# Optimization experiments

Measured on AMD Instinct MI355X. Metric: run time of the kernel, lower is better.

Reference implementation:

```python
import jax, jax.numpy as jnp
import numpy as np

N = 50000   # nodes
E = 800000  # edges (before self loops)
NEG_SLOPE = 0.2
EPS_BN = 1e-5
EPS_SM = 1e-16  # PyG softmax denominator epsilon


def gat_conv(x, src, dst, W, att_src, att_dst, bias, heads, ch):
    n = x.shape[0]
    xh = (x @ W).reshape(n, heads, ch)                       # [N,H,C]
    a_src = jnp.sum(xh * att_src, axis=-1)                   # [N,H]
    a_dst = jnp.sum(xh * att_dst, axis=-1)                   # [N,H]
    e = a_src[src] + a_dst[dst]                              # [E,H]
    e = jax.nn.leaky_relu(e, NEG_SLOPE)
    m = jax.ops.segment_max(e, dst, num_segments=n)          # segment softmax
    ex = jnp.exp(e - m[dst])
    denom = jax.ops.segment_sum(ex, dst, num_segments=n)
    alpha = ex / (denom[dst] + EPS_SM)                       # [E,H]
    msg = alpha[:, :, None] * xh[src]                        # [E,H,C]
    out = jax.ops.segment_sum(msg, dst, num_segments=n)      # [N,H,C]
    return out.reshape(n, heads * ch) + bias


def batch_norm(x, gamma, beta):
    mu = jnp.mean(x, axis=0)
    var = jnp.mean((x - mu) ** 2, axis=0)
    return (x - mu) * jax.lax.rsqrt(var + EPS_BN) * gamma + beta


def setup_inputs() -> dict:
    key = jax.random.key(0)
    ks = jax.random.split(key, 16)
    d = {}
    d['x'] = jax.random.normal(ks[0], (N, 128), jnp.float32)
    d['edge_index'] = jax.random.randint(ks[1], (2, E), 0, N, dtype=jnp.int64)
    d['W1'] = jax.random.normal(ks[2], (128, 256), jnp.float32) * 0.1
    d['as1'] = jax.random.normal(ks[3], (2, 128), jnp.float32) * 0.1
    d['ad1'] = jax.random.normal(ks[4], (2, 128), jnp.float32) * 0.1
    d['b1'] = jax.random.normal(ks[5], (256,), jnp.float32) * 0.1
    d['g1'] = jnp.ones((256,), jnp.float32)
    d['be1'] = jnp.zeros((256,), jnp.float32)
    d['W2'] = jax.random.normal(ks[6], (256, 128), jnp.float32) * 0.1
    d['as2'] = jax.random.normal(ks[7], (2, 64), jnp.float32) * 0.1
    d['ad2'] = jax.random.normal(ks[8], (2, 64), jnp.float32) * 0.1
    d['b2'] = jax.random.normal(ks[9], (128,), jnp.float32) * 0.1
    d['g2'] = jnp.ones((128,), jnp.float32)
    d['be2'] = jnp.zeros((128,), jnp.float32)
    d['W3'] = jax.random.normal(ks[10], (128, 128), jnp.float32) * 0.1
    d['as3'] = jax.random.normal(ks[11], (2, 64), jnp.float32) * 0.1
    d['ad3'] = jax.random.normal(ks[12], (2, 64), jnp.float32) * 0.1
    d['b3'] = jax.random.normal(ks[13], (128,), jnp.float32) * 0.1
    d['lw'] = jax.random.normal(ks[14], (128, 64), jnp.float32) * 0.1
    d['lb'] = jnp.zeros((64,), jnp.float32)
    return d


def reference(x, edge_index, W1, as1, ad1, b1, g1, be1,
              W2, as2, ad2, b2, g2, be2,
              W3, as3, ad3, b3, lw, lb):
    # add self loops (PyG GATConv default add_self_loops=True)
    loops = jnp.arange(N, dtype=edge_index.dtype)
    src = jnp.concatenate([edge_index[0], loops])
    dst = jnp.concatenate([edge_index[1], loops])

    h = jax.nn.relu(gat_conv(x, src, dst, W1, as1, ad1, b1, 2, 128))   # [N,256]
    h = batch_norm(h, g1, be1)
    h = jax.nn.relu(gat_conv(h, src, dst, W2, as2, ad2, b2, 2, 64))    # [N,128]
    h = batch_norm(h, g2, be2)
    h = jax.nn.relu(gat_conv(h, src, dst, W3, as3, ad3, b3, 2, 64))    # [N,128]
    return h @ lw + lb                                                 # [N,64]
```

## Files before the change

kernel.cpp:

```cpp
#include <hip/hip_runtime.h>
#include <hip/hip_bf16.h>

#define NEG_SLOPE 0.2f
#define EPS_BN 1e-5f
#define EPS_SM 1e-16f
#define CAP 128

typedef __bf16 bf16x8 __attribute__((ext_vector_type(8)));
typedef __bf16 bf16x4 __attribute__((ext_vector_type(4)));
typedef float floatx4 __attribute__((ext_vector_type(4)));

__device__ __forceinline__ float leaky(float x) { return x > 0.f ? x : NEG_SLOPE * x; }

__global__ void k_init(const int* __restrict__ ei, int* __restrict__ flag,
                       int* __restrict__ zbase, int zwords, int e,
                       const float* __restrict__ W1, const float* __restrict__ as1,
                       const float* __restrict__ ad1, float* __restrict__ wsd) {
    if (blockIdx.x == 0) {
        __shared__ int cnt_s[256];
        int i = threadIdx.x;
        int nz = (2 * i + 1 < 2 * e && ei[2 * i + 1] != 0) ? 1 : 0;
        cnt_s[i] = nz;
        __syncthreads();
        for (int off = 128; off > 0; off >>= 1) {
            if (i < off) cnt_s[i] += cnt_s[i + off];
            __syncthreads();
        }
        if (i == 0) *flag = (cnt_s[0] < 128) ? 1 : 0;
        return;
    }
    if (blockIdx.x == 65) {
        int k = threadIdx.x;
        if (k < 128) {
            const float* wr = W1 + (size_t)k * 256;
            float s0 = 0.f, s1 = 0.f, d0 = 0.f, d1 = 0.f;
            for (int c = 0; c < 128; ++c) {
                float w0 = wr[c], w1 = wr[128 + c];
                s0 += w0 * as1[c];
                s1 += w1 * as1[128 + c];
                d0 += w0 * ad1[c];
                d1 += w1 * ad1[128 + c];
            }
            wsd[k] = s0; wsd[128 + k] = s1; wsd[256 + k] = d0; wsd[384 + k] = d1;
        }
        return;
    }
    int g = (blockIdx.x - 1) * 256 + threadIdx.x;
    const int stride = 64 * 256;
    for (int k = g; k < zwords; k += stride) zbase[k] = 0;
}

__global__ void k_hist_wconv(const int* __restrict__ ei, const int* __restrict__ flag,
                             int* __restrict__ deg, int* __restrict__ col, int e, int ebase,
                             const float* __restrict__ W1, __bf16* __restrict__ Wb1,
                             const float* __restrict__ W2, __bf16* __restrict__ Wb2,
                             const float* __restrict__ W3, __bf16* __restrict__ Wb3) {
    int g = threadIdx.x + blockIdx.x * blockDim.x;
    if (g < e) {
        bool is64 = (*flag) != 0;
        int s = is64 ? ei[2 * g] : ei[g];
        int d = is64 ? ei[2 * (e + g)] : ei[e + g];
        int r = atomicAdd(&deg[d], 1);
        if (r < CAP) col[((size_t)d << 7) + r] = s;
    } else {
        int idx = g - ebase;
        if (idx >= 0 && idx < 32768) {
            int mm = idx >> 7, kk = idx & 127;
            Wb1[idx] = (__bf16)W1[(size_t)kk * 256 + mm];
        } else if (idx < 65536) {
            int i2 = idx - 32768;
            int mm = i2 >> 8, kk = i2 & 255;
            Wb2[i2] = (__bf16)W2[(size_t)kk * 128 + mm];
        } else if (idx < 81920) {
            int i3 = idx - 65536;
            int mm = i3 >> 7, kk = i3 & 127;
            Wb3[i3] = (__bf16)W3[(size_t)kk * 128 + mm];
        }
    }
}

__global__ __launch_bounds__(256) void k_pre(const float* __restrict__ x,
                                             const float* __restrict__ wsd,
                                             __bf16* __restrict__ xb,
                                             float* __restrict__ asp,
                                             float* __restrict__ adp, int n) {
    __shared__ float ws[4][128];
    for (int i = threadIdx.x; i < 512; i += 256) ws[i >> 7][i & 127] = wsd[i];
    __syncthreads();
    const int lane = threadIdx.x & 63, widx = threadIdx.x >> 6;
    const int sub = lane & 7;
    const int node = blockIdx.x * 32 + widx * 8 + (lane >> 3);
    if (node >= n) return;
    const int c0 = sub * 16;
    const float* xp = x + (size_t)node * 128 + c0;
    float xv[16];
#pragma unroll
    for (int q = 0; q < 4; ++q) {
        float4 v = *reinterpret_cast<const float4*>(xp + q * 4);
        xv[q * 4 + 0] = v.x; xv[q * 4 + 1] = v.y; xv[q * 4 + 2] = v.z; xv[q * 4 + 3] = v.w;
    }
    float s0 = 0.f, s1 = 0.f, d0 = 0.f, d1 = 0.f;
#pragma unroll
    for (int i = 0; i < 16; ++i) {
        float xi = xv[i];
        int c = c0 + i;
        s0 += xi * ws[0][c]; s1 += xi * ws[1][c];
        d0 += xi * ws[2][c]; d1 += xi * ws[3][c];
    }
#pragma unroll
    for (int off = 1; off <= 4; off <<= 1) {
        s0 += __shfl_xor(s0, off); s1 += __shfl_xor(s1, off);
        d0 += __shfl_xor(d0, off); d1 += __shfl_xor(d1, off);
    }
    bf16x8 b0, b1;
#pragma unroll
    for (int i = 0; i < 8; ++i) { b0[i] = (__bf16)xv[i]; b1[i] = (__bf16)xv[8 + i]; }
    __bf16* po = xb + (size_t)node * 128 + c0;
    *reinterpret_cast<bf16x8*>(po) = b0;
    *reinterpret_cast<bf16x8*>(po + 8) = b1;
    if (sub == 0) {
        *reinterpret_cast<float2*>(asp + 2 * node) = make_float2(s0, s1);
        *reinterpret_cast<float2*>(adp + 2 * node) = make_float2(d0, d1);
    }
}

__global__ __launch_bounds__(256) void k_agg_in(const __bf16* __restrict__ xb,
                                                const float* __restrict__ asrc,
                                                const float* __restrict__ adst,
                                                const int* __restrict__ degv,
                                                const int* __restrict__ col,
                                                __bf16* __restrict__ aggv, int n) {
    __shared__ float4 slots[4][80];
    const int widx = threadIdx.x >> 6;
    const int node = blockIdx.x * 4 + widx;
    const int lane = threadIdx.x & 63;
    if (node >= n) return;
    const int t = lane & 15;
    const int g = lane >> 4;
    if (lane >= 48) slots[widx][lane + 16] = make_float4(0.f, 0.f, 0.f, 0.f);
    const char* xbt = (const char*)xb + t * 16;
    const int* crow = col + ((size_t)node << 7);
    const int deg = min(degv[node], CAP);
    const float2 adv = *reinterpret_cast<const float2*>(adst + 2 * node);
    const float2 asv = *reinterpret_cast<const float2*>(asrc + 2 * node);
    const float es0 = leaky(asv.x + adv.x), es1 = leaky(asv.y + adv.y);
    float a0[8] = {}, a1[8] = {};
    float d0 = 0.f, d1 = 0.f;
    for (int base = 0; base < deg; base += 64) {
        const int cnt = min(64, deg - base);
        float4 sv = make_float4(0.f, 0.f, 0.f, 0.f);
        if (lane < cnt) {
            int s = crow[base + lane];
            float2 av = *reinterpret_cast<const float2*>(asrc + 2 * s);
            float w0 = __expf(leaky(av.x + adv.x));
            float w1 = __expf(leaky(av.y + adv.y));
            d0 += w0; d1 += w1;
            sv = make_float4(__int_as_float(s * 256), w0, w1, 0.f);
        }
        slots[widx][lane] = sv;
        for (int j = g; j < cnt; j += 16) {
            float4 s0 = slots[widx][j];
            float4 s1 = slots[widx][j + 4];
            float4 s2 = slots[widx][j + 8];
            float4 s3 = slots[widx][j + 12];
            bf16x8 v0 = *reinterpret_cast<const bf16x8*>(xbt + (unsigned)__float_as_int(s0.x));
            bf16x8 v1 = *reinterpret_cast<const bf16x8*>(xbt + (unsigned)__float_as_int(s1.x));
            bf16x8 v2 = *reinterpret_cast<const bf16x8*>(xbt + (unsigned)__float_as_int(s2.x));
            bf16x8 v3 = *reinterpret_cast<const bf16x8*>(xbt + (unsigned)__float_as_int(s3.x));
#pragma unroll
            for (int q = 0; q < 8; ++q) {
                float f0 = (float)v0[q], f1 = (float)v1[q], f2 = (float)v2[q], f3 = (float)v3[q];
                a0[q] += s0.y * f0 + s1.y * f1 + s2.y * f2 + s3.y * f3;
                a1[q] += s0.z * f0 + s1.z * f1 + s2.z * f2 + s3.z * f3;
            }
        }
    }
#pragma unroll
    for (int off = 1; off <= 32; off <<= 1) {
        d0 += __shfl_xor(d0, off);
        d1 += __shfl_xor(d1, off);
    }
#pragma unroll
    for (int q = 0; q < 8; ++q) {
#pragma unroll
        for (int off = 16; off < 64; off <<= 1) {
            a0[q] += __shfl_xor(a0[q], off);
            a1[q] += __shfl_xor(a1[q], off);
        }
    }
    float exs0 = __expf(es0), exs1 = __expf(es1);
    d0 += exs0; d1 += exs1;
    {
        bf16x8 v = *reinterpret_cast<const bf16x8*>(xbt + (size_t)node * 256);
#pragma unroll
        for (int q = 0; q < 8; ++q) {
            a0[q] += exs0 * (float)v[q];
            a1[q] += exs1 * (float)v[q];
        }
    }
    float i0 = 1.0f / (d0 + EPS_SM), i1 = 1.0f / (d1 + EPS_SM);
    if (g == 0) {
        bf16x8 st0, st1;
#pragma unroll
        for (int q = 0; q < 8; ++q) {
            st0[q] = (__bf16)(a0[q] * i0);
            st1[q] = (__bf16)(a1[q] * i1);
        }
        __bf16* po = aggv + (size_t)node * 256 + t * 8;
        *reinterpret_cast<bf16x8*>(po) = st0;
        *reinterpret_cast<bf16x8*>(po + 128) = st1;
    }
}

__global__ __launch_bounds__(256) void k_gemm_ar(const __bf16* __restrict__ A,
                                                 const __bf16* __restrict__ Bt,
                                                 const float* __restrict__ bias,
                                                 __bf16* __restrict__ Cb, int n) {
    __shared__ __align__(16) __bf16 As[128][72];
    __shared__ __align__(16) __bf16 Bs[128][72];
    const int row0 = blockIdx.y * 128, col0 = blockIdx.x * 128;
    const int h = col0 >> 7;
    const int lane = threadIdx.x & 63, w = threadIdx.x >> 6;
    const int m = lane & 15, quad = lane >> 4;
    floatx4 acc[2][8];
#pragma unroll
    for (int i = 0; i < 2; ++i)
#pragma unroll
        for (int j = 0; j < 8; ++j) acc[i][j] = (floatx4)0.f;
    const int sr = threadIdx.x >> 1;
    const int sk = (threadIdx.x & 1) * 32;
    for (int kc = 0; kc < 128; kc += 64) {
        {
            int grow = row0 + sr;
            if (grow < n) {
                const __bf16* p = A + (size_t)grow * 256 + h * 128 + kc + sk;
#pragma unroll
                for (int q = 0; q < 4; ++q)
                    *reinterpret_cast<bf16x8*>(&As[sr][sk + q * 8]) =
                        *reinterpret_cast<const bf16x8*>(p + q * 8);
            } else {
#pragma unroll
                for (int q = 0; q < 4; ++q)
                    *reinterpret_cast<bf16x8*>(&As[sr][sk + q * 8]) = (bf16x8)(__bf16)0.f;
            }
        }
        {
            const __bf16* p = Bt + (size_t)(col0 + sr) * 128 + kc + sk;
#pragma unroll
            for (int q = 0; q < 4; ++q)
                *reinterpret_cast<bf16x8*>(&Bs[sr][sk + q * 8]) =
                    *reinterpret_cast<const bf16x8*>(p + q * 8);
        }
        __syncthreads();
#pragma unroll
        for (int ks = 0; ks < 64; ks += 32) {
            bf16x8 a0 = *reinterpret_cast<const bf16x8*>(&As[w * 32 + m][ks + quad * 8]);
            bf16x8 a1 = *reinterpret_cast<const bf16x8*>(&As[w * 32 + 16 + m][ks + quad * 8]);
#pragma unroll
            for (int nt = 0; nt < 8; ++nt) {
                bf16x8 b = *reinterpret_cast<const bf16x8*>(&Bs[nt * 16 + m][ks + quad * 8]);
                acc[0][nt] = __builtin_amdgcn_mfma_f32_16x16x32_bf16(a0, b, acc[0][nt], 0, 0, 0);
                acc[1][nt] = __builtin_amdgcn_mfma_f32_16x16x32_bf16(a1, b, acc[1][nt], 0, 0, 0);
            }
        }
        __syncthreads();
    }
#pragma unroll
    for (int mt = 0; mt < 2; ++mt)
#pragma unroll
        for (int nt = 0; nt < 8; ++nt)
#pragma unroll
            for (int r = 0; r < 4; ++r) {
                int row = row0 + w * 32 + mt * 16 + quad * 4 + r;
                int c = col0 + nt * 16 + m;
                if (row < n)
                    Cb[(size_t)row * 256 + c] = (__bf16)fmaxf(acc[mt][nt][r] + bias[c], 0.f);
            }
}

template <int K, int LC, bool BF16IN, int NT>
__global__ __launch_bounds__(256) void k_gemm(const void* __restrict__ Ain,
                                              const __bf16* __restrict__ Bt,
                                              __bf16* __restrict__ Cb, int n, int M,
                                              const float* __restrict__ bnsums,
                                              const float* __restrict__ gam,
                                              const float* __restrict__ bet,
                                              const float* __restrict__ att_s,
                                              const float* __restrict__ att_d,
                                              float* __restrict__ asrc,
                                              float* __restrict__ adst) {
    __shared__ __align__(16) __bf16 As[128][72];
    __shared__ __align__(16) __bf16 Bs[NT * 16][72];
    __shared__ float sc_lds[K], sh_lds[K];
    const int row0 = blockIdx.y * 128, col0 = blockIdx.x * (NT * 16);
    const int lane = threadIdx.x & 63, w = threadIdx.x >> 6;
    const int m = lane & 15, quad = lane >> 4;

    if (bnsums) {
        for (int c = threadIdx.x; c < K; c += 256) {
            float mean = bnsums[c] / n;
            float var = bnsums[256 + c] / n - mean * mean;
            float sc = gam[c] * rsqrtf(var + EPS_BN);
            sc_lds[c] = sc;
            sh_lds[c] = bet[c] - mean * sc;
        }
        __syncthreads();
    }

    floatx4 acc[2][NT];
#pragma unroll
    for (int i = 0; i < 2; ++i)
#pragma unroll
        for (int j = 0; j < NT; ++j) acc[i][j] = (floatx4)0.f;

    const int sr = threadIdx.x >> 1;
    const int sk = (threadIdx.x & 1) * 32;

    for (int kc = 0; kc < K; kc += 64) {
        {
            int grow = row0 + sr;
            if (grow < n) {
                if (BF16IN) {
                    const __bf16* p = (const __bf16*)Ain + (size_t)grow * K + kc + sk;
#pragma unroll
                    for (int q = 0; q < 4; ++q) {
                        bf16x8 vv = *reinterpret_cast<const bf16x8*>(p + q * 8);
                        if (bnsums) {
                            int c = kc + sk + q * 8;
                            bf16x8 r;
#pragma unroll
                            for (int e2 = 0; e2 < 8; ++e2)
                                r[e2] = (__bf16)((float)vv[e2] * sc_lds[c + e2] + sh_lds[c + e2]);
                            vv = r;
                        }
                        *reinterpret_cast<bf16x8*>(&As[sr][sk + q * 8]) = vv;
                    }
                } else {
                    const float* p = (const float*)Ain + (size_t)grow * K + kc + sk;
#pragma unroll
                    for (int q = 0; q < 8; ++q) {
                        float4 v = *reinterpret_cast<const float4*>(p + q * 4);
                        bf16x4 cv = {(__bf16)v.x, (__bf16)v.y, (__bf16)v.z, (__bf16)v.w};
                        *reinterpret_cast<bf16x4*>(&As[sr][sk + q * 4]) = cv;
                    }
                }
            } else {
#pragma unroll
                for (int q = 0; q < 4; ++q)
                    *reinterpret_cast<bf16x8*>(&As[sr][sk + q * 8]) = (bf16x8)(__bf16)0.f;
            }
        }
        if (NT == 8) {
            const __bf16* p = Bt + (size_t)(col0 + sr) * K + kc + sk;
#pragma unroll
            for (int q = 0; q < 4; ++q)
                *reinterpret_cast<bf16x8*>(&Bs[sr][sk + q * 8]) =
                    *reinterpret_cast<const bf16x8*>(p + q * 8);
        } else {
            int sr4 = threadIdx.x >> 2, sk4 = (threadIdx.x & 3) * 16;
            const __bf16* p = Bt + (size_t)(col0 + sr4) * K + kc + sk4;
            *reinterpret_cast<bf16x8*>(&Bs[sr4][sk4]) = *reinterpret_cast<const bf16x8*>(p);
            *reinterpret_cast<bf16x8*>(&Bs[sr4][sk4 + 8]) = *reinterpret_cast<const bf16x8*>(p + 8);
        }
        __syncthreads();
#pragma unroll
        for (int ks = 0; ks < 64; ks += 32) {
            bf16x8 a0 = *reinterpret_cast<const bf16x8*>(&As[w * 32 + m][ks + quad * 8]);
            bf16x8 a1 = *reinterpret_cast<const bf16x8*>(&As[w * 32 + 16 + m][ks + quad * 8]);
#pragma unroll
            for (int nt = 0; nt < NT; ++nt) {
                bf16x8 b = *reinterpret_cast<const bf16x8*>(&Bs[nt * 16 + m][ks + quad * 8]);
                acc[0][nt] = __builtin_amdgcn_mfma_f32_16x16x32_bf16(a0, b, acc[0][nt], 0, 0, 0);
                acc[1][nt] = __builtin_amdgcn_mfma_f32_16x16x32_bf16(a1, b, acc[1][nt], 0, 0, 0);
            }
        }
        __syncthreads();
    }
#pragma unroll
    for (int mt = 0; mt < 2; ++mt)
#pragma unroll
        for (int nt = 0; nt < NT; ++nt)
#pragma unroll
            for (int r = 0; r < 4; ++r) {
                int row = row0 + w * 32 + mt * 16 + quad * 4 + r;
                if (row < n) Cb[(size_t)row * M + col0 + nt * 16 + m] = (__bf16)acc[mt][nt][r];
            }
    {
        float asv[NT], adv[NT];
#pragma unroll
        for (int nt = 0; nt < NT; ++nt) {
            int c = col0 + nt * 16 + m;
            asv[nt] = att_s[c];
            adv[nt] = att_d[c];
        }
        const int h = (col0 >> LC) & 1;
#pragma unroll
        for (int mt = 0; mt < 2; ++mt)
#pragma unroll
            for (int r = 0; r < 4; ++r) {
                int row = row0 + w * 32 + mt * 16 + quad * 4 + r;
                float pa = 0.f, pb = 0.f;
#pragma unroll
                for (int nt = 0; nt < NT; ++nt) {
                    float v = acc[mt][nt][r];
                    pa += v * asv[nt];
                    pb += v * adv[nt];
                }
#pragma unroll
                for (int off = 1; off <= 8; off <<= 1) {
                    pa += __shfl_xor(pa, off);
                    pb += __shfl_xor(pb, off);
                }
                if (m == 0 && row < n) {
                    asrc[2 * row + h] = pa;
                    adst[2 * row + h] = pb;
                }
            }
    }
}

__global__ __launch_bounds__(256) void k_lin(const float* __restrict__ A,
                                             const float* __restrict__ lw,
                                             const float* __restrict__ lb,
                                             float* __restrict__ out, int n) {
    __shared__ __align__(16) __bf16 Ahi[64][136];
    __shared__ __align__(16) __bf16 Alo[64][136];
    __shared__ __align__(16) __bf16 Bhi[64][136];
    const int row0 = blockIdx.x * 64;
    const int lane = threadIdx.x & 63, w = threadIdx.x >> 6;
    const int m = lane & 15, quad = lane >> 4;
    floatx4 acc[4];
#pragma unroll
    for (int i = 0; i < 4; ++i) acc[i] = (floatx4)0.f;
    {
        int sr = threadIdx.x >> 2, sk0 = (threadIdx.x & 3) * 32;
        int grow = row0 + sr;
#pragma unroll
        for (int q = 0; q < 8; ++q) {
            float4 v = make_float4(0.f, 0.f, 0.f, 0.f);
            if (grow < n) v = *reinterpret_cast<const float4*>(A + (size_t)grow * 128 + sk0 + q * 4);
            float vv[4] = {v.x, v.y, v.z, v.w};
#pragma unroll
            for (int i = 0; i < 4; ++i) {
                __bf16 h = (__bf16)vv[i];
                Ahi[sr][sk0 + q * 4 + i] = h;
                Alo[sr][sk0 + q * 4 + i] = (__bf16)(vv[i] - (float)h);
            }
        }
    }
    {
        int k0 = threadIdx.x >> 1, m0 = (threadIdx.x & 1) * 32;
#pragma unroll
        for (int q = 0; q < 8; ++q) {
            float4 v = *reinterpret_cast<const float4*>(lw + (size_t)k0 * 64 + m0 + q * 4);
            float vv[4] = {v.x, v.y, v.z, v.w};
#pragma unroll
            for (int i = 0; i < 4; ++i) Bhi[m0 + q * 4 + i][k0] = (__bf16)vv[i];
        }
    }
    __syncthreads();
#pragma unroll
    for (int ks = 0; ks < 128; ks += 32) {
        bf16x8 ah = *reinterpret_cast<const bf16x8*>(&Ahi[w * 16 + m][ks + quad * 8]);
        bf16x8 al = *reinterpret_cast<const bf16x8*>(&Alo[w * 16 + m][ks + quad * 8]);
#pragma unroll
        for (int nt = 0; nt < 4; ++nt) {
            bf16x8 bh = *reinterpret_cast<const bf16x8*>(&Bhi[nt * 16 + m][ks + quad * 8]);
            acc[nt] = __builtin_amdgcn_mfma_f32_16x16x32_bf16(ah, bh, acc[nt], 0, 0, 0);
            acc[nt] = __builtin_amdgcn_mfma_f32_16x16x32_bf16(al, bh, acc[nt], 0, 0, 0);
        }
    }
#pragma unroll
    for (int nt = 0; nt < 4; ++nt)
#pragma unroll
        for (int r = 0; r < 4; ++r) {
            int row = row0 + w * 16 + quad * 4 + r;
            int c = nt * 16 + m;
            if (row < n) out[(size_t)row * 64 + c] = acc[nt][r] + lb[c];
        }
}

template <int C, bool OUTBF16>
__global__ __launch_bounds__(256) void k_agg(const __bf16* __restrict__ xh,
                                             const float* __restrict__ asrc,
                                             const float* __restrict__ adst,
                                             const int* __restrict__ degv,
                                             const int* __restrict__ col,
                                             const float* __restrict__ bias,
                                             void* __restrict__ outv, int n) {
    constexpr int F = 2 * C;
    constexpr int G = F / 8;
    constexpr int NG = 64 / G;
    constexpr int GSH = (G == 32) ? 5 : 4;
    __shared__ float4 slots[4][80];
    const int widx = threadIdx.x >> 6;
    const int node = blockIdx.x * 4 + widx;
    const int lane = threadIdx.x & 63;
    if (node >= n) return;
    const int t = lane & (G - 1);
    const int g = lane >> GSH;
    const bool h1 = (t * 8) >= C;
    if (lane >= 48) slots[widx][lane + 16] = make_float4(0.f, 0.f, 0.f, 0.f);
    const int* crow = col + ((size_t)node << 7);
    const int deg = min(degv[node], CAP);
    const float2 adv = *reinterpret_cast<const float2*>(adst + 2 * node);
    const float2 asv = *reinterpret_cast<const float2*>(asrc + 2 * node);
    const float es0 = leaky(asv.x + adv.x), es1 = leaky(asv.y + adv.y);
    float acc[8] = {};
    float d0 = 0.f, d1 = 0.f;
    for (int base = 0; base < deg; base += 64) {
        const int cnt = min(64, deg - base);
        float4 sv = make_float4(0.f, 0.f, 0.f, 0.f);
        if (lane < cnt) {
            int s = crow[base + lane];
            float2 av = *reinterpret_cast<const float2*>(asrc + 2 * s);
            float w0 = __expf(leaky(av.x + adv.x));
            float w1 = __expf(leaky(av.y + adv.y));
            d0 += w0; d1 += w1;
            sv = make_float4(__int_as_float(s * (F * 2)), w0, w1, 0.f);
        }
        slots[widx][lane] = sv;
        for (int j = g; j < cnt; j += 4 * NG) {
            float4 s0 = slots[widx][j];
            float4 s1 = slots[widx][j + NG];
            float4 s2 = slots[widx][j + 2 * NG];
            float4 s3 = slots[widx][j + 3 * NG];
            const char* xb = (const char*)xh;
            bf16x8 v0 = *reinterpret_cast<const bf16x8*>(xb + (unsigned)__float_as_int(s0.x) + t * 16);
            bf16x8 v1 = *reinterpret_cast<const bf16x8*>(xb + (unsigned)__float_as_int(s1.x) + t * 16);
            bf16x8 v2 = *reinterpret_cast<const bf16x8*>(xb + (unsigned)__float_as_int(s2.x) + t * 16);
            bf16x8 v3 = *reinterpret_cast<const bf16x8*>(xb + (unsigned)__float_as_int(s3.x) + t * 16);
            float w0 = h1 ? s0.z : s0.y;
            float w1 = h1 ? s1.z : s1.y;
            float w2 = h1 ? s2.z : s2.y;
            float w3 = h1 ? s3.z : s3.y;
#pragma unroll
            for (int q = 0; q < 8; ++q)
                acc[q] += w0 * (float)v0[q] + w1 * (float)v1[q] +
                          w2 * (float)v2[q] + w3 * (float)v3[q];
        }
    }
#pragma unroll
    for (int off = 1; off <= 32; off <<= 1) {
        d0 += __shfl_xor(d0, off);
        d1 += __shfl_xor(d1, off);
    }
#pragma unroll
    for (int q = 0; q < 8; ++q) {
#pragma unroll
        for (int off = G; off < 64; off <<= 1) acc[q] += __shfl_xor(acc[q], off);
    }
    float exs0 = __expf(es0), exs1 = __expf(es1);
    d0 += exs0; d1 += exs1;
    {
        float ws = h1 ? exs1 : exs0;
        bf16x8 v = *reinterpret_cast<const bf16x8*>(xh + (size_t)node * F + t * 8);
#pragma unroll
        for (int q = 0; q < 8; ++q) acc[q] += ws * (float)v[q];
    }
    float inv = 1.0f / ((h1 ? d1 : d0) + EPS_SM);
    float o[8];
#pragma unroll
    for (int q = 0; q < 8; ++q) o[q] = fmaxf(acc[q] * inv + bias[t * 8 + q], 0.f);
    if (g == 0) {
        if constexpr (OUTBF16) {
            __bf16* po = (__bf16*)outv + (size_t)node * F + t * 8;
            bf16x8 st;
#pragma unroll
            for (int q = 0; q < 8; ++q) st[q] = (__bf16)o[q];
            *reinterpret_cast<bf16x8*>(po) = st;
        } else {
            float* po = (float*)outv + (size_t)node * F + t * 8;
            *reinterpret_cast<float4*>(po) = make_float4(o[0], o[1], o[2], o[3]);
            *reinterpret_cast<float4*>(po + 4) = make_float4(o[4], o[5], o[6], o[7]);
        }
    }
}

template <typename T>
__global__ void k_bn_stats(const T* __restrict__ x, float* __restrict__ sums,
                           float* __restrict__ sqs, int n, int f) {
    int c = threadIdx.x;
    float s = 0.f, q = 0.f;
    for (int r = blockIdx.x; r < n; r += gridDim.x) {
        float v = (float)x[(size_t)r * f + c];
        s += v; q += v * v;
    }
    atomicAdd(&sums[c], s);
    atomicAdd(&sqs[c], q);
}

extern "C" void kernel_launch(void* const* d_in, const int* in_sizes, int n_in,
                              void* d_out, int out_size, void* d_ws, size_t ws_size,
                              hipStream_t stream) {
    const float* x   = (const float*)d_in[0];
    const int*   ei  = (const int*)d_in[1];
    const float* W1  = (const float*)d_in[2];
    const float* as1 = (const float*)d_in[3];
    const float* ad1 = (const float*)d_in[4];
    const float* b1  = (const float*)d_in[5];
    const float* g1  = (const float*)d_in[6];
    const float* be1 = (const float*)d_in[7];
    const float* W2  = (const float*)d_in[8];
    const float* as2 = (const float*)d_in[9];
    const float* ad2 = (const float*)d_in[10];
    const float* b2  = (const float*)d_in[11];
    const float* g2  = (const float*)d_in[12];
    const float* be2 = (const float*)d_in[13];
    const float* W3  = (const float*)d_in[14];
    const float* as3 = (const float*)d_in[15];
    const float* ad3 = (const float*)d_in[16];
    const float* b3  = (const float*)d_in[17];
    const float* lw  = (const float*)d_in[18];
    const float* lb  = (const float*)d_in[19];
    float* outp = (float*)d_out;

    const int n = in_sizes[0] / 128;
    const int e = in_sizes[1] / 2;

    char* w = (char*)d_ws;
    size_t off = 0;
    auto alloc = [&](size_t bytes) -> void* {
        void* p = w + off;
        off += (bytes + 255) & ~(size_t)255;
        return p;
    };
    __bf16* xhb = (__bf16*)alloc((size_t)n * 256 * 2);
    __bf16* h1b = (__bf16*)alloc((size_t)n * 256 * 2);
    __bf16* h2b = (__bf16*)alloc((size_t)n * 128 * 2);
    float*  h3f = (float*)alloc((size_t)n * 128 * 4);
    int* colb   = (int*)alloc((size_t)n * CAP * 4);
    __bf16* xb  = (__bf16*)alloc((size_t)n * 128 * 2);
    __bf16* Wb1 = (__bf16*)alloc(256 * 128 * 2);
    __bf16* Wb2 = (__bf16*)alloc(128 * 256 * 2);
    __bf16* Wb3 = (__bf16*)alloc(128 * 128 * 2);
    float* wsd  = (float*)alloc(512 * 4);
    int* flag   = (int*)alloc(256);
    float* as1p = (float*)alloc((size_t)n * 2 * 4);
    float* ad1p = (float*)alloc((size_t)n * 2 * 4);
    float* as2p = (float*)alloc((size_t)n * 2 * 4);
    float* ad2p = (float*)alloc((size_t)n * 2 * 4);
    float* as3p = (float*)alloc((size_t)n * 2 * 4);
    float* ad3p = (float*)alloc((size_t)n * 2 * 4);
    char* zb_begin = (char*)(w + off);
    int* deg    = (int*)alloc((size_t)n * 4);
    float* bn1  = (float*)alloc(512 * 4);
    float* bn2  = (float*)alloc(512 * 4);
    char* zb_end = (char*)(w + off);
    const int zwords = (int)((zb_end - zb_begin) / 4);

    k_init<<<66, 256, 0, stream>>>(ei, flag, (int*)zb_begin, zwords, e, W1, as1, ad1, wsd);

    const int ebase = ((e + 255) / 256) * 256;
    const int histblocks = ebase / 256 + 320;
    k_hist_wconv<<<histblocks, 256, 0, stream>>>(ei, flag, deg, colb, e, ebase,
                                                 W1, Wb1, W2, Wb2, W3, Wb3);

    const int nwb = (n + 3) / 4;
    const int nrow = (n + 127) / 128;

    k_pre<<<(n + 31) / 32, 256, 0, stream>>>(x, wsd, xb, as1p, ad1p, n);
    k_agg_in<<<nwb, 256, 0, stream>>>(xb, as1p, ad1p, deg, colb, xhb, n);
    k_gemm_ar<<<dim3(2, nrow), 256, 0, stream>>>(xhb, Wb1, b1, h1b, n);
    k_bn_stats<__bf16><<<256, 256, 0, stream>>>(h1b, bn1, bn1 + 256, n, 256);

    k_gemm<256, 6, true, 4><<<dim3(2, nrow), 256, 0, stream>>>(
        h1b, Wb2, xhb, n, 128, bn1, g1, be1, as2, ad2, as2p, ad2p);
    k_agg<64, true><<<nwb, 256, 0, stream>>>(xhb, as2p, ad2p, deg, colb, b2, h2b, n);
    k_bn_stats<__bf16><<<256, 128, 0, stream>>>(h2b, bn2, bn2 + 256, n, 128);

    k_gemm<128, 6, true, 4><<<dim3(2, nrow), 256, 0, stream>>>(
        h2b, Wb3, xhb, n, 128, bn2, g2, be2, as3, ad3, as3p, ad3p);
    k_agg<64, false><<<nwb, 256, 0, stream>>>(xhb, as3p, ad3p, deg, colb, b3, h3f, n);

    k_lin<<<(n + 63) / 64, 256, 0, stream>>>(h3f, lw, lb, outp, n);
}
```

Before: 472.6 us.

## Fuse pre-pass into hist kernel, BN1 stats into GEMM epilogue, split agg slots

Merges the k_pre input-conversion pass into the histogram/weight-conversion launch and folds the first batch-norm statistics into the k_gemm_ar epilogue via shuffle reduction and atomics, removing two launches and one full reread of h1. The aggregation kernels now store neighbor offsets and weights in separate shared arrays and pad with the node's own index, which removes float-int bitcasts. They also load the self-loop feature vector early so it overlaps the gather. The atomic accumulation makes the BN sums order-dependent, and k_pre's __syncthreads now sits inside a kernel where some threads return early, which relies on whole blocks taking the same branch.

New measurement: 440.1 us. -6.9%, faster.

```diff
diff --git a/kernel.cpp b/kernel.cpp
--- a/kernel.cpp
+++ b/kernel.cpp
@@ -54,7 +54,10 @@
                              int* __restrict__ deg, int* __restrict__ col, int e, int ebase,
                              const float* __restrict__ W1, __bf16* __restrict__ Wb1,
                              const float* __restrict__ W2, __bf16* __restrict__ Wb2,
-                             const float* __restrict__ W3, __bf16* __restrict__ Wb3) {
+                             const float* __restrict__ W3, __bf16* __restrict__ Wb3,
+                             const float* __restrict__ x, const float* __restrict__ wsd,
+                             __bf16* __restrict__ xb, float* __restrict__ asp,
+                             float* __restrict__ adp, int n) {
     int g = threadIdx.x + blockIdx.x * blockDim.x;
     if (g < e) {
         bool is64 = (*flag) != 0;
@@ -62,34 +65,32 @@
         int d = is64 ? ei[2 * (e + g)] : ei[e + g];
         int r = atomicAdd(&deg[d], 1);
         if (r < CAP) col[((size_t)d << 7) + r] = s;
-    } else {
-        int idx = g - ebase;
-        if (idx >= 0 && idx < 32768) {
+        return;
+    }
+    int idx = g - ebase;
+    if (idx < 0) return;
+    if (idx < 81920) {
+        if (idx < 32768) {
             int mm = idx >> 7, kk = idx & 127;
             Wb1[idx] = (__bf16)W1[(size_t)kk * 256 + mm];
         } else if (idx < 65536) {
             int i2 = idx - 32768;
             int mm = i2 >> 8, kk = i2 & 255;
             Wb2[i2] = (__bf16)W2[(size_t)kk * 128 + mm];
-        } else if (idx < 81920) {
+        } else {
             int i3 = idx - 65536;
             int mm = i3 >> 7, kk = i3 & 127;
             Wb3[i3] = (__bf16)W3[(size_t)kk * 128 + mm];
         }
-    }
-}
-
-__global__ __launch_bounds__(256) void k_pre(const float* __restrict__ x,
-                                             const float* __restrict__ wsd,
-                                             __bf16* __restrict__ xb,
-                                             float* __restrict__ asp,
-                                             float* __restrict__ adp, int n) {
+        return;
+    }
+    int p = idx - 81920;
     __shared__ float ws[4][128];
     for (int i = threadIdx.x; i < 512; i += 256) ws[i >> 7][i & 127] = wsd[i];
     __syncthreads();
     const int lane = threadIdx.x & 63, widx = threadIdx.x >> 6;
     const int sub = lane & 7;
-    const int node = blockIdx.x * 32 + widx * 8 + (lane >> 3);
+    const int node = (p >> 8) * 32 + widx * 8 + (lane >> 3);
     if (node >= n) return;
     const int c0 = sub * 16;
     const float* xp = x + (size_t)node * 128 + c0;
@@ -130,48 +131,49 @@
                                                 const int* __restrict__ degv,
                                                 const int* __restrict__ col,
                                                 __bf16* __restrict__ aggv, int n) {
-    __shared__ float4 slots[4][80];
+    __shared__ int sA[4][80];
+    __shared__ float2 sW[4][80];
     const int widx = threadIdx.x >> 6;
     const int node = blockIdx.x * 4 + widx;
     const int lane = threadIdx.x & 63;
     if (node >= n) return;
     const int t = lane & 15;
     const int g = lane >> 4;
-    if (lane >= 48) slots[widx][lane + 16] = make_float4(0.f, 0.f, 0.f, 0.f);
+    const int selfoff = node * 256;
+    if (lane >= 48) { sA[widx][lane + 16] = selfoff; sW[widx][lane + 16] = make_float2(0.f, 0.f); }
     const char* xbt = (const char*)xb + t * 16;
     const int* crow = col + ((size_t)node << 7);
     const int deg = min(degv[node], CAP);
     const float2 adv = *reinterpret_cast<const float2*>(adst + 2 * node);
     const float2 asv = *reinterpret_cast<const float2*>(asrc + 2 * node);
     const float es0 = leaky(asv.x + adv.x), es1 = leaky(asv.y + adv.y);
+    bf16x8 vself = *reinterpret_cast<const bf16x8*>(xbt + selfoff);
     float a0[8] = {}, a1[8] = {};
     float d0 = 0.f, d1 = 0.f;
     for (int base = 0; base < deg; base += 64) {
         const int cnt = min(64, deg - base);
-        float4 sv = make_float4(0.f, 0.f, 0.f, 0.f);
+        int s = (lane < cnt) ? crow[base + lane] : node;
+        sA[widx][lane] = s * 256;
+        float2 av = *reinterpret_cast<const float2*>(asrc + 2 * s);
+        float w0 = 0.f, w1 = 0.f;
         if (lane < cnt) {
-            int s = crow[base + lane];
-            float2 av = *reinterpret_cast<const float2*>(asrc + 2 * s);
-            float w0 = __expf(leaky(av.x + adv.x));
-            float w1 = __expf(leaky(av.y + adv.y));
+            w0 = __expf(leaky(av.x + adv.x));
+            w1 = __expf(leaky(av.y + adv.y));
             d0 += w0; d1 += w1;
-            sv = make_float4(__int_as_float(s * 256), w0, w1, 0.f);
-        }
-        slots[widx][lane] = sv;
+        }
+        sW[widx][lane] = make_float2(w0, w1);
         for (int j = g; j < cnt; j += 16) {
-            float4 s0 = slots[widx][j];
-            float4 s1 = slots[widx][j + 4];
-            float4 s2 = slots[widx][j + 8];
-            float4 s3 = slots[widx][j + 12];
-            bf16x8 v0 = *reinterpret_cast<const bf16x8*>(xbt + (unsigned)__float_as_int(s0.x));
-            bf16x8 v1 = *reinterpret_cast<const bf16x8*>(xbt + (unsigned)__float_as_int(s1.x));
-            bf16x8 v2 = *reinterpret_cast<const bf16x8*>(xbt + (unsigned)__float_as_int(s2.x));
-            bf16x8 v3 = *reinterpret_cast<const bf16x8*>(xbt + (unsigned)__float_as_int(s3.x));
+            int o0 = sA[widx][j], o1 = sA[widx][j + 4], o2 = sA[widx][j + 8], o3 = sA[widx][j + 12];
+            bf16x8 v0 = *reinterpret_cast<const bf16x8*>(xbt + o0);
+            bf16x8 v1 = *reinterpret_cast<const bf16x8*>(xbt + o1);
+            bf16x8 v2 = *reinterpret_cast<const bf16x8*>(xbt + o2);
+            bf16x8 v3 = *reinterpret_cast<const bf16x8*>(xbt + o3);
+            float2 x0 = sW[widx][j], x1 = sW[widx][j + 4], x2 = sW[widx][j + 8], x3 = sW[widx][j + 12];
 #pragma unroll
             for (int q = 0; q < 8; ++q) {
                 float f0 = (float)v0[q], f1 = (float)v1[q], f2 = (float)v2[q], f3 = (float)v3[q];
-                a0[q] += s0.y * f0 + s1.y * f1 + s2.y * f2 + s3.y * f3;
-                a1[q] += s0.z * f0 + s1.z * f1 + s2.z * f2 + s3.z * f3;
+                a0[q] += x0.x * f0 + x1.x * f1 + x2.x * f2 + x3.x * f3;
+                a1[q] += x0.y * f0 + x1.y * f1 + x2.y * f2 + x3.y * f3;
             }
         }
     }
@@ -190,13 +192,10 @@
     }
     float exs0 = __expf(es0), exs1 = __expf(es1);
     d0 += exs0; d1 += exs1;
-    {
-        bf16x8 v = *reinterpret_cast<const bf16x8*>(xbt + (size_t)node * 256);
-#pragma unroll
-        for (int q = 0; q < 8; ++q) {
-            a0[q] += exs0 * (float)v[q];
-            a1[q] += exs1 * (float)v[q];
-        }
+#pragma unroll
+    for (int q = 0; q < 8; ++q) {
+        a0[q] += exs0 * (float)vself[q];
+        a1[q] += exs1 * (float)vself[q];
     }
     float i0 = 1.0f / (d0 + EPS_SM), i1 = 1.0f / (d1 + EPS_SM);
     if (g == 0) {
@@ -215,7 +214,8 @@
 __global__ __launch_bounds__(256) void k_gemm_ar(const __bf16* __restrict__ A,
                                                  const __bf16* __restrict__ Bt,
                                                  const float* __restrict__ bias,
-                                                 __bf16* __restrict__ Cb, int n) {
+                                                 __bf16* __restrict__ Cb,
+                                                 float* __restrict__ bnsums, int n) {
     __shared__ __align__(16) __bf16 As[128][72];
     __shared__ __align__(16) __bf16 Bs[128][72];
     const int row0 = blockIdx.y * 128, col0 = blockIdx.x * 128;
@@ -265,17 +265,39 @@
         }
         __syncthreads();
     }
-#pragma unroll
-    for (int mt = 0; mt < 2; ++mt)
-#pragma unroll
-        for (int nt = 0; nt < 8; ++nt)
+    float* redS = reinterpret_cast<float*>(As);
+    float* redQ = redS + 512;
+#pragma unroll
+    for (int nt = 0; nt < 8; ++nt) {
+        float bsv = bias[col0 + nt * 16 + m];
+        float ssum = 0.f, ssq = 0.f;
+#pragma unroll
+        for (int mt = 0; mt < 2; ++mt)
 #pragma unroll
             for (int r = 0; r < 4; ++r) {
                 int row = row0 + w * 32 + mt * 16 + quad * 4 + r;
-                int c = col0 + nt * 16 + m;
-                if (row < n)
-                    Cb[(size_t)row * 256 + c] = (__bf16)fmaxf(acc[mt][nt][r] + bias[c], 0.f);
-            }
+                float v = 0.f;
+                if (row < n) {
+                    v = fmaxf(acc[mt][nt][r] + bsv, 0.f);
+                    Cb[(size_t)row * 256 + col0 + nt * 16 + m] = (__bf16)v;
+                }
+                ssum += v; ssq += v * v;
+            }
+        ssum += __shfl_xor(ssum, 16); ssum += __shfl_xor(ssum, 32);
+        ssq  += __shfl_xor(ssq, 16);  ssq  += __shfl_xor(ssq, 32);
+        if (quad == 0) {
+            redS[w * 128 + nt * 16 + m] = ssum;
+            redQ[w * 128 + nt * 16 + m] = ssq;
+        }
+    }
+    __syncthreads();
+    if (threadIdx.x < 128) {
+        int c = threadIdx.x;
+        float s = redS[c] + redS[128 + c] + redS[256 + c] + redS[384 + c];
+        float q2 = redQ[c] + redQ[128 + c] + redQ[256 + c] + redQ[384 + c];
+        atomicAdd(&bnsums[col0 + c], s);
+        atomicAdd(&bnsums[256 + col0 + c], q2);
+    }
 }
 
 template <int K, int LC, bool BF16IN, int NT>
@@ -492,7 +514,8 @@
     constexpr int G = F / 8;
     constexpr int NG = 64 / G;
     constexpr int GSH = (G == 32) ? 5 : 4;
-    __shared__ float4 slots[4][80];
+    __shared__ int sA[4][80];
+    __shared__ float2 sW[4][80];
     const int widx = threadIdx.x >> 6;
     const int node = blockIdx.x * 4 + widx;
     const int lane = threadIdx.x & 63;
@@ -500,40 +523,40 @@
     const int t = lane & (G - 1);
     const int g = lane >> GSH;
     const bool h1 = (t * 8) >= C;
-    if (lane >= 48) slots[widx][lane + 16] = make_float4(0.f, 0.f, 0.f, 0.f);
+    const int selfoff = node * (F * 2);
+    if (lane >= 48) { sA[widx][lane + 16] = selfoff; sW[widx][lane + 16] = make_float2(0.f, 0.f); }
+    const char* xbt = (const char*)xh + t * 16;
     const int* crow = col + ((size_t)node << 7);
     const int deg = min(degv[node], CAP);
     const float2 adv = *reinterpret_cast<const float2*>(adst + 2 * node);
     const float2 asv = *reinterpret_cast<const float2*>(asrc + 2 * node);
     const float es0 = leaky(asv.x + adv.x), es1 = leaky(asv.y + adv.y);
+    bf16x8 vself = *reinterpret_cast<const bf16x8*>(xbt + selfoff);
     float acc[8] = {};
     float d0 = 0.f, d1 = 0.f;
     for (int base = 0; base < deg; base += 64) {
         const int cnt = min(64, deg - base);
-        float4 sv = make_float4(0.f, 0.f, 0.f, 0.f);
+        int s = (lane < cnt) ? crow[base + lane] : node;
+        sA[widx][lane] = s * (F * 2);
+        float2 av = *reinterpret_cast<const float2*>(asrc + 2 * s);
+        float w0 = 0.f, w1 = 0.f;
         if (lane < cnt) {
-            int s = crow[base + lane];
-            float2 av = *reinterpret_cast<const float2*>(asrc + 2 * s);
-            float w0 = __expf(leaky(av.x + adv.x));
-            float w1 = __expf(leaky(av.y + adv.y));
+            w0 = __expf(leaky(av.x + adv.x));
+            w1 = __expf(leaky(av.y + adv.y));
             d0 += w0; d1 += w1;
-            sv = make_float4(__int_as_float(s * (F * 2)), w0, w1, 0.f);
-        }
-        slots[widx][lane] = sv;
+        }
+        sW[widx][lane] = make_float2(w0, w1);
         for (int j = g; j < cnt; j += 4 * NG) {
-            float4 s0 = slots[widx][j];
-            float4 s1 = slots[widx][j + NG];
-            float4 s2 = slots[widx][j + 2 * NG];
-            float4 s3 = slots[widx][j + 3 * NG];
-            const char* xb = (const char*)xh;
-            bf16x8 v0 = *reinterpret_cast<const bf16x8*>(xb + (unsigned)__float_as_int(s0.x) + t * 16);
-            bf16x8 v1 = *reinterpret_cast<const bf16x8*>(xb + (unsigned)__float_as_int(s1.x) + t * 16);
-            bf16x8 v2 = *reinterpret_cast<const bf16x8*>(xb + (unsigned)__float_as_int(s2.x) + t * 16);
-            bf16x8 v3 = *reinterpret_cast<const bf16x8*>(xb + (unsigned)__float_as_int(s3.x) + t * 16);
-            float w0 = h1 ? s0.z : s0.y;
-            float w1 = h1 ? s1.z : s1.y;
-            float w2 = h1 ? s2.z : s2.y;
-            float w3 = h1 ? s3.z : s3.y;
+            int o0 = sA[widx][j], o1 = sA[widx][j + NG], o2 = sA[widx][j + 2 * NG], o3 = sA[widx][j + 3 * NG];
+            bf16x8 v0 = *reinterpret_cast<const bf16x8*>(xbt + o0);
+            bf16x8 v1 = *reinterpret_cast<const bf16x8*>(xbt + o1);
+            bf16x8 v2 = *reinterpret_cast<const bf16x8*>(xbt + o2);
+            bf16x8 v3 = *reinterpret_cast<const bf16x8*>(xbt + o3);
+            float2 x0 = sW[widx][j], x1 = sW[widx][j + NG], x2 = sW[widx][j + 2 * NG], x3 = sW[widx][j + 3 * NG];
+            float w0 = h1 ? x0.y : x0.x;
+            float w1 = h1 ? x1.y : x1.x;
+            float w2 = h1 ? x2.y : x2.x;
+            float w3 = h1 ? x3.y : x3.x;
 #pragma unroll
             for (int q = 0; q < 8; ++q)
                 acc[q] += w0 * (float)v0[q] + w1 * (float)v1[q] +
@@ -554,9 +577,8 @@
     d0 += exs0; d1 += exs1;
     {
         float ws = h1 ? exs1 : exs0;
-        bf16x8 v = *reinterpret_cast<const bf16x8*>(xh + (size_t)node * F + t * 8);
-#pragma unroll
-        for (int q = 0; q < 8; ++q) acc[q] += ws * (float)v[q];
+#pragma unroll
+        for (int q = 0; q < 8; ++q) acc[q] += ws * (float)vself[q];
     }
     float inv = 1.0f / ((h1 ? d1 : d0) + EPS_SM);
     float o[8];
@@ -652,17 +674,17 @@
     k_init<<<66, 256, 0, stream>>>(ei, flag, (int*)zb_begin, zwords, e, W1, as1, ad1, wsd);
 
     const int ebase = ((e + 255) / 256) * 256;
-    const int histblocks = ebase / 256 + 320;
+    const int preblocks = (n + 31) / 32;
+    const int histblocks = ebase / 256 + 320 + preblocks;
     k_hist_wconv<<<histblocks, 256, 0, stream>>>(ei, flag, deg, colb, e, ebase,
-                                                 W1, Wb1, W2, Wb2, W3, Wb3);
+                                                 W1, Wb1, W2, Wb2, W3, Wb3,
+                                                 x, wsd, xb, as1p, ad1p, n);
 
     const int nwb = (n + 3) / 4;
     const int nrow = (n + 127) / 128;
 
-    k_pre<<<(n + 31) / 32, 256, 0, stream>>>(x, wsd, xb, as1p, ad1p, n);
     k_agg_in<<<nwb, 256, 0, stream>>>(xb, as1p, ad1p, deg, colb, xhb, n);
-    k_gemm_ar<<<dim3(2, nrow), 256, 0, stream>>>(xhb, Wb1, b1, h1b, n);
-    k_bn_stats<__bf16><<<256, 256, 0, stream>>>(h1b, bn1, bn1 + 256, n, 256);
+    k_gemm_ar<<<dim3(2, nrow), 256, 0, stream>>>(xhb, Wb1, b1, h1b, bn1, n);
 
     k_gemm<256, 6, true, 4><<<dim3(2, nrow), 256, 0, stream>>>(
         h1b, Wb2, xhb, n, 128, bn1, g1, be1, as2, ad2, as2p, ad2p);
```
